# Kernel optimization log

Hardware: AMD Instinct MI355X
Metric: run time of the kernel (lower is better)

Reference implementation:

```python
import jax, jax.numpy as jnp
import numpy as np


def _seg_softmax(e, seg, n):
    m = jax.ops.segment_max(e, seg, num_segments=n)
    ex = jnp.exp(e - m[seg])
    s = jax.ops.segment_sum(ex, seg, num_segments=n)
    return ex / (s[seg] + 1e-16)


def _gat_conv(x, src, dst, ea, W, a_s, a_d, We, a_e, b, heads, C, concat, N):
    # PyG GATConv math (eval mode, no dropout)
    h = (x @ W).reshape(N, heads, C)                    # [N,H,C]
    he = (ea @ We).reshape(-1, heads, C)                # [Ef,H,C]
    al = jnp.sum(h * a_s, -1)[src] + jnp.sum(h * a_d, -1)[dst] + jnp.sum(he * a_e, -1)
    al = jax.nn.leaky_relu(al, 0.2)                     # [Ef,H]
    alpha = _seg_softmax(al, dst, N)
    out = jax.ops.segment_sum(alpha[:, :, None] * h[src], dst, num_segments=N)
    out = out.reshape(N, heads * C) if concat else out.mean(1)
    return out + b


def _ln(x, g, b):
    mu = x.mean(-1, keepdims=True)
    v = x.var(-1, keepdims=True)
    return (x - mu) / jnp.sqrt(v + 1e-5) * g + b


def setup_inputs() -> dict:
    key = jax.random.key(0)
    ks = jax.random.split(key, 20)
    B, L, E_PER = 512, 64, 4
    N = B * L
    E = N * E_PER
    x = jax.random.normal(ks[0], (N, 55), jnp.float32)
    # within-graph random edges (each graph is a contiguous block of L nodes)
    off = (jnp.arange(E) // (L * E_PER)) * L
    src = off + jax.random.randint(ks[1], (E,), 0, L)
    dst = off + jax.random.randint(ks[2], (E,), 0, L)
    edge_index = jnp.stack([src, dst])
    edge_attr = jax.random.uniform(ks[3], (E, 6), dtype=jnp.float32)
    node_gid = jnp.arange(N) // L
    food_ids = jax.random.randint(ks[4], (B,), 0, 29)
    p = lambda i, shape: jax.random.normal(ks[i], shape, jnp.float32) * 0.05
    return dict(
        x=x, edge_attr=edge_attr, edge_index=edge_index, node_gid=node_gid, food_ids=food_ids,
        W1=p(5, (55, 1024)), as1=p(6, (4, 256)), ad1=p(7, (4, 256)),
        We1=p(8, (6, 1024)), ae1=p(9, (4, 256)), b1=jnp.zeros((1024,), jnp.float32),
        g1=jnp.ones((1024,), jnp.float32), be1=jnp.zeros((1024,), jnp.float32),
        W2=p(10, (1024, 256)), as2=p(11, (1, 256)), ad2=p(12, (1, 256)),
        We2=p(13, (6, 256)), ae2=p(14, (1, 256)), b2=jnp.zeros((256,), jnp.float32),
        g2=jnp.ones((256,), jnp.float32), be2=jnp.zeros((256,), jnp.float32),
        Wa=p(15, (256, 256)), va=p(16, (256,)), emb=p(17, (29, 256)))


def reference(x, edge_attr, edge_index, node_gid, food_ids,
              W1, as1, ad1, We1, ae1, b1, g1, be1,
              W2, as2, ad2, We2, ae2, b2, g2, be2,
              Wa, va, emb):
    N = x.shape[0]
    B = food_ids.shape[0]
    src, dst = edge_index[0], edge_index[1]
    # add self loops; self-loop edge_attr = mean of incoming edge attrs (PyG fill_value='mean')
    ones = jnp.ones((src.shape[0],), x.dtype)
    deg = jax.ops.segment_sum(ones, dst, num_segments=N)
    mean_ea = jax.ops.segment_sum(edge_attr, dst, num_segments=N) / jnp.maximum(deg, 1.0)[:, None]
    loop = jnp.arange(N)
    src_f = jnp.concatenate([src, loop])
    dst_f = jnp.concatenate([dst, loop])
    ea_f = jnp.concatenate([edge_attr, mean_ea], 0)
    # GATEncoder
    h = _gat_conv(x, src_f, dst_f, ea_f, W1, as1, ad1, We1, ae1, b1, 4, 256, True, N)
    h = jax.nn.relu(_ln(h, g1, be1))
    h = _gat_conv(h, src_f, dst_f, ea_f, W2, as2, ad2, We2, ae2, b2, 1, 256, False, N)
    h = _ln(h, g2, be2)                                  # [N,256]
    # per-graph attention over nodes, then attention-weighted max-pool
    scores = jnp.tanh(h @ Wa) @ va                       # [N]
    attn = _seg_softmax(scores, node_gid, B)             # [N]
    hw = h * attn[:, None]
    drug_fea = jax.ops.segment_max(hw, node_gid, num_segments=B)[:, None, :]  # [B,1,256]
    food_fea = emb[food_ids][:, None, :]                 # [B,1,256]
    return drug_fea, food_fea, attn
```

## Files before the change

kernel.cpp:

```cpp
#include <hip/hip_runtime.h>
#include <cstdint>
#include <cstddef>


#define LEAKY_SLOPE 0.2f

typedef __attribute__((ext_vector_type(8))) _Float16 half8;
typedef __attribute__((ext_vector_type(4))) float facc4;

__global__ void k_prep_w(const float* __restrict__ W1, const float* __restrict__ W2,
                         const float* __restrict__ Wa,
                         const float* __restrict__ We1, const float* __restrict__ ae1,
                         const float* __restrict__ We2, const float* __restrict__ ae2,
                         const float* __restrict__ as1, const float* __restrict__ ad1,
                         _Float16* __restrict__ w1t, _Float16* __restrict__ w2t,
                         _Float16* __restrict__ wat, float* __restrict__ fold) {
    int idx = blockIdx.x * blockDim.x + threadIdx.x;
    if (idx < 1024 * 64) {
        int c = idx >> 6, k = idx & 63;
        w1t[idx] = (k < 55) ? (_Float16)W1[(size_t)k * 1024 + c] : (_Float16)0.f;
        return;
    }
    idx -= 1024 * 64;
    if (idx < 256 * 1024) {
        int c = idx >> 10, k = idx & 1023;
        w2t[idx] = (_Float16)W2[(size_t)k * 256 + c];
        return;
    }
    idx -= 256 * 1024;
    if (idx < 256 * 256) {
        int c = idx >> 8, k = idx & 255;
        int dst = ((c >> 4) * 8 + (k >> 5)) * 512 + ((c & 15) + 16 * ((k >> 3) & 3)) * 8 + (k & 7);
        wat[dst] = (_Float16)Wa[(size_t)k * 256 + c];
        return;
    }
    int t = idx - 256 * 256;
    if (t < 24) {
        int k = t >> 2, h = t & 3;
        float s = 0.f;
        for (int c = 0; c < 256; ++c) s += We1[k * 1024 + h * 256 + c] * ae1[h * 256 + c];
        fold[t] = s;
    } else if (t < 30) {
        int k = t - 24;
        float s = 0.f;
        for (int c = 0; c < 256; ++c) s += We2[k * 256 + c] * ae2[c];
        fold[32 + k] = s;
    } else if (t >= 64 && t < 284) {
        int i = t - 64, k = i >> 2, h = i & 3;
        float s = 0.f;
        for (int c = 0; c < 256; ++c) s += W1[k * 1024 + h * 256 + c] * as1[h * 256 + c];
        fold[64 + i] = s;
    } else if (t >= 320 && t < 540) {
        int i = t - 320, k = i >> 2, h = i & 3;
        float s = 0.f;
        for (int c = 0; c < 256; ++c) s += W1[k * 1024 + h * 256 + c] * ad1[h * 256 + c];
        fold[320 + i] = s;
    }
}

__global__ void k_prep_x(const float* __restrict__ x, const float* __restrict__ wa1,
                         const float* __restrict__ wd1, _Float16* __restrict__ xbf,
                         float* __restrict__ ss1, float* __restrict__ sd1, int N) {
    int idx = blockIdx.x * blockDim.x + threadIdx.x;
    if (idx < N * 64) {
        int n = idx >> 6, k = idx & 63;
        _Float16 v = (k < 55) ? (_Float16)x[(size_t)n * 55 + k] : (_Float16)0.f;
        int g = n >> 6, nl = n & 63;
        size_t dst = (size_t)g * 4096 +
                     (((k >> 4) * 2 + (nl >> 5)) * 512 +
                      ((k & 15) + 16 * ((nl >> 3) & 3)) * 8 + (nl & 7));
        xbf[dst] = v;
        return;
    }
    int n = idx - N * 64;
    if (n >= N) return;
    float a0 = 0, a1 = 0, a2 = 0, a3 = 0, d0 = 0, d1 = 0, d2 = 0, d3 = 0;
    for (int k = 0; k < 55; ++k) {
        float xv = x[(size_t)n * 55 + k];
        float4 wa = *reinterpret_cast<const float4*>(&wa1[k * 4]);
        float4 wd = *reinterpret_cast<const float4*>(&wd1[k * 4]);
        a0 += xv * wa.x; a1 += xv * wa.y; a2 += xv * wa.z; a3 += xv * wa.w;
        d0 += xv * wd.x; d1 += xv * wd.y; d2 += xv * wd.z; d3 += xv * wd.w;
    }
    *reinterpret_cast<float4*>(&ss1[n * 4]) = make_float4(a0, a1, a2, a3);
    *reinterpret_cast<float4*>(&sd1[n * 4]) = make_float4(d0, d1, d2, d3);
}

__global__ __launch_bounds__(256) void k_graph_csr(
    const int* __restrict__ ei, const float* __restrict__ ea,
    const float* __restrict__ we1, const float* __restrict__ we2,
    int* __restrict__ coff, int* __restrict__ eid,
    float* __restrict__ ead1, float* __restrict__ ead2, int E, int B) {
    __shared__ int degL[64];
    __shared__ float meaL[64][6];
    __shared__ int cs[65];
    __shared__ int fillL[64];
    int g = blockIdx.x;
    int ng = g * 64;
    int e0 = g * 256;
    int tid = threadIdx.x;
    if (tid < 64) {
        degL[tid] = 0; fillL[tid] = 0;
#pragma unroll
        for (int k = 0; k < 6; ++k) meaL[tid][k] = 0.f;
    }
    __syncthreads();
    int eg = e0 + tid;
    int dst = ei[E + eg];
    int dl = dst - ng;
    atomicAdd(&degL[dl], 1);
#pragma unroll
    for (int k = 0; k < 6; ++k) atomicAdd(&meaL[dl][k], ea[(size_t)eg * 6 + k]);
    __syncthreads();
    if (tid < 64) {
        int v = degL[tid] + 1;
        int incl = v;
#pragma unroll
        for (int o = 1; o < 64; o <<= 1) {
            int up = __shfl_up(incl, o);
            if (tid >= o) incl += up;
        }
        cs[tid + 1] = incl;
        if (tid == 0) cs[0] = 0;
        coff[ng + tid] = g * 320 + (incl - v);
        if (g == B - 1 && tid == 63) coff[ng + 64] = (g + 1) * 320;
    }
    __syncthreads();
    {
        float v[4] = {};
        float v2 = 0.f;
        const float* eap = ea + (size_t)eg * 6;
#pragma unroll
        for (int k = 0; k < 6; ++k) {
            float a = eap[k];
#pragma unroll
            for (int h = 0; h < 4; ++h) v[h] += a * we1[k * 4 + h];
            v2 += a * we2[k];
        }
#pragma unroll
        for (int h = 0; h < 4; ++h) ead1[(size_t)eg * 4 + h] = v[h];
        ead2[eg] = v2;
        int pos = cs[dl] + atomicAdd(&fillL[dl], 1);
        eid[g * 320 + pos] = eg;
    }
    if (tid < 64) {
        float inv = 1.f / fmaxf((float)degL[tid], 1.f);
        float v[4] = {};
        float v2 = 0.f;
#pragma unroll
        for (int k = 0; k < 6; ++k) {
            float a = meaL[tid][k] * inv;
#pragma unroll
            for (int h = 0; h < 4; ++h) v[h] += a * we1[k * 4 + h];
            v2 += a * we2[k];
        }
        int se = E + ng + tid;
#pragma unroll
        for (int h = 0; h < 4; ++h) ead1[(size_t)se * 4 + h] = v[h];
        ead2[se] = v2;
        int pos = cs[tid] + atomicAdd(&fillL[tid], 1);
        eid[g * 320 + pos] = se;
    }
}

__global__ __launch_bounds__(512) void k_pbuild1(
    const _Float16* __restrict__ xbf,
    const int* __restrict__ coff, const int* __restrict__ eid, const int* __restrict__ ei,
    const float* __restrict__ ead1, const float* __restrict__ ss1,
    const float* __restrict__ sd1,
    _Float16* __restrict__ XA, int ldxa, int E, int g0) {
    __shared__ _Float16 Pm[4][64 * 64];
    __shared__ float llds[384][4];
    __shared__ int slds[384];
    int g = blockIdx.x;
    int ng = (g0 + g) * 64;
    int lr0 = g * 64;
    int tid = threadIdx.x;
    int lane = tid & 63, wid = tid >> 6;
    int l15 = lane & 15, l4 = lane >> 4;
    for (int i = tid; i < 4 * 64 * 64 / 8; i += 512)
        *reinterpret_cast<int4*>(&Pm[0][0] + i * 8) = int4{0, 0, 0, 0};
    int pbase = coff[ng];
    int pcnt = coff[ng + 64] - pbase;
    if (pcnt > 384) pcnt = 384;
    for (int p = tid; p < pcnt; p += 512) {
        int e = eid[pbase + p];
        int s, d;
        if (e < E) { s = ei[e]; d = ei[E + e]; } else { s = e - E; d = s; }
        slds[p] = s - ng;
        float4 sv = *reinterpret_cast<const float4*>(&ss1[s * 4]);
        float4 dv = *reinterpret_cast<const float4*>(&sd1[d * 4]);
        float4 ev = *reinterpret_cast<const float4*>(&ead1[(size_t)e * 4]);
        float v0 = sv.x + dv.x + ev.x, v1 = sv.y + dv.y + ev.y;
        float v2 = sv.z + dv.z + ev.z, v3 = sv.w + dv.w + ev.w;
        llds[p][0] = (v0 > 0.f) ? v0 : LEAKY_SLOPE * v0;
        llds[p][1] = (v1 > 0.f) ? v1 : LEAKY_SLOPE * v1;
        llds[p][2] = (v2 > 0.f) ? v2 : LEAKY_SLOPE * v2;
        llds[p][3] = (v3 > 0.f) ? v3 : LEAKY_SLOPE * v3;
    }
    __syncthreads();
    if (tid < 256) {
        int dst = tid >> 2, h = tid & 3;
        int p0 = coff[ng + dst] - pbase, p1 = coff[ng + dst + 1] - pbase;
        float m = -1e30f;
        for (int p = p0; p < p1; ++p) m = fmaxf(m, llds[p][h]);
        float sm = 0.f;
        for (int p = p0; p < p1; ++p) sm += expf(llds[p][h] - m);
        float iv = 1.f / (sm + 1e-16f);
        for (int p = p0; p < p1; ++p) {
            int src = slds[p];
            int pos = dst * 64 + (((src >> 3) ^ (dst & 7)) << 3) + (src & 7);
            Pm[h][pos] = (_Float16)((float)Pm[h][pos] + expf(llds[p][h] - m) * iv);
        }
    }
    __syncthreads();
    int head = wid >> 1, fjh = wid & 1;
    const _Float16* xg = xbf + (size_t)(g0 + g) * 4096;
    facc4 acc[4][2] = {};
#pragma unroll
    for (int kk = 0; kk < 2; ++kk) {
        half8 af[4], bf[2];
#pragma unroll
        for (int f = 0; f < 4; ++f) {
            int arow = f * 16 + l15;
            af[f] = *reinterpret_cast<const half8*>(
                &Pm[head][arow * 64 + (((kk * 4 + l4) ^ (arow & 7)) << 3)]);
        }
#pragma unroll
        for (int f = 0; f < 2; ++f)
            bf[f] = *reinterpret_cast<const half8*>(
                xg + (((fjh * 2 + f) * 2 + kk) * 512 + lane * 8));
#pragma unroll
        for (int fi = 0; fi < 4; ++fi)
#pragma unroll
            for (int fj = 0; fj < 2; ++fj)
                acc[fi][fj] = __builtin_amdgcn_mfma_f32_16x16x32_f16(
                    af[fi], bf[fj], acc[fi][fj], 0, 0, 0);
    }
#pragma unroll
    for (int fi = 0; fi < 4; ++fi)
#pragma unroll
        for (int fj = 0; fj < 2; ++fj)
#pragma unroll
            for (int i = 0; i < 4; ++i) {
                int r = fi * 16 + l4 * 4 + i;
                int k2 = fjh * 32 + fj * 16 + l15;
                XA[((size_t)head * ldxa + lr0 + r) * 64 + k2] = (_Float16)acc[fi][fj][i];
            }
}

__global__ __launch_bounds__(256) void k_gemm_heads(
    const _Float16* __restrict__ XA, int ldxa, const _Float16* __restrict__ w1t,
    _Float16* __restrict__ hpre) {
    int h = blockIdx.z;
    const _Float16* A = XA + (size_t)h * ldxa * 64;
    const _Float16* BT = w1t + (size_t)h * 256 * 64;
    __shared__ _Float16 As[128 * 64];
    __shared__ _Float16 Bs[128 * 64];
    int tid = threadIdx.x;
    int lane = tid & 63, wid = tid >> 6;
    int wr = wid >> 1, wc = wid & 1;
    int l15 = lane & 15, l4 = lane >> 4;
    int r0 = blockIdx.y * 128, c0 = blockIdx.x * 128;
    facc4 acc[4][4] = {};
#pragma unroll
    for (int i = 0; i < 4; ++i) {
        int ch = tid + 256 * i;
        int row = ch >> 3, col16 = ch & 7;
        int sw = col16 ^ (row & 7);
        *reinterpret_cast<int4*>(&As[row * 64 + sw * 8]) =
            *reinterpret_cast<const int4*>(A + (size_t)(r0 + row) * 64 + col16 * 8);
        *reinterpret_cast<int4*>(&Bs[row * 64 + sw * 8]) =
            *reinterpret_cast<const int4*>(BT + (size_t)(c0 + row) * 64 + col16 * 8);
    }
    __syncthreads();
#pragma unroll
    for (int kk = 0; kk < 2; ++kk) {
        half8 af[4], bf[4];
#pragma unroll
        for (int f = 0; f < 4; ++f) {
            int arow = wr * 64 + f * 16 + l15;
            int ac = (kk * 4 + l4) ^ (arow & 7);
            af[f] = *reinterpret_cast<const half8*>(&As[arow * 64 + ac * 8]);
            int brow = wc * 64 + f * 16 + l15;
            int bc = (kk * 4 + l4) ^ (brow & 7);
            bf[f] = *reinterpret_cast<const half8*>(&Bs[brow * 64 + bc * 8]);
        }
#pragma unroll
        for (int fi = 0; fi < 4; ++fi)
#pragma unroll
            for (int fj = 0; fj < 4; ++fj)
                acc[fi][fj] = __builtin_amdgcn_mfma_f32_16x16x32_f16(
                    af[fi], bf[fj], acc[fi][fj], 0, 0, 0);
    }
#pragma unroll
    for (int fi = 0; fi < 4; ++fi)
#pragma unroll
        for (int fj = 0; fj < 4; ++fj)
#pragma unroll
            for (int i = 0; i < 4; ++i) {
                int r = r0 + wr * 64 + fi * 16 + l4 * 4 + i;
                int cc = h * 256 + c0 + wc * 64 + fj * 16 + l15;
                hpre[(size_t)r * 1024 + cc] = (_Float16)acc[fi][fj][i];
            }
}

__global__ __launch_bounds__(256) void k_ln1(
    const _Float16* __restrict__ hpre, const float* __restrict__ b1,
    const float* __restrict__ g1, const float* __restrict__ be1,
    _Float16* __restrict__ hln) {
    int row = blockIdx.x * 4 + (threadIdx.x >> 6);
    int lane = threadIdx.x & 63;
    const _Float16* src = hpre + (size_t)row * 1024;
    float v[16];
    half8 h0 = *reinterpret_cast<const half8*>(src + lane * 8);
    half8 h1 = *reinterpret_cast<const half8*>(src + 512 + lane * 8);
    float lsum = 0.f, lsq = 0.f;
#pragma unroll
    for (int j = 0; j < 8; ++j) {
        v[j] = (float)h0[j] + b1[lane * 8 + j];
        v[8 + j] = (float)h1[j] + b1[512 + lane * 8 + j];
    }
#pragma unroll
    for (int j = 0; j < 16; ++j) { lsum += v[j]; lsq += v[j] * v[j]; }
    for (int o = 32; o; o >>= 1) { lsum += __shfl_xor(lsum, o); lsq += __shfl_xor(lsq, o); }
    float mu = lsum * (1.f / 1024.f);
    float var = lsq * (1.f / 1024.f) - mu * mu;
    float rstd = rsqrtf(var + 1e-5f);
    half8 o0, o1;
#pragma unroll
    for (int j = 0; j < 8; ++j) {
        int c = lane * 8 + j;
        o0[j] = (_Float16)fmaxf((v[j] - mu) * rstd * g1[c] + be1[c], 0.f);
    }
#pragma unroll
    for (int j = 0; j < 8; ++j) {
        int c = 512 + lane * 8 + j;
        o1[j] = (_Float16)fmaxf((v[8 + j] - mu) * rstd * g1[c] + be1[c], 0.f);
    }
    *reinterpret_cast<half8*>(hln + (size_t)row * 1024 + lane * 8) = o0;
    *reinterpret_cast<half8*>(hln + (size_t)row * 1024 + 512 + lane * 8) = o1;
}

__global__ __launch_bounds__(512) void k_gemm2(
    const _Float16* __restrict__ A, const _Float16* __restrict__ BT,
    _Float16* __restrict__ h2f) {
    __shared__ _Float16 As[128 * 64];
    __shared__ _Float16 Bs[256 * 64];
    int tid = threadIdx.x;
    int lane = tid & 63, wid = tid >> 6;
    int wr = wid >> 2, wc = wid & 3;
    int l15 = lane & 15, l4 = lane >> 4;
    int r0 = blockIdx.x * 128;
    facc4 acc[4][4] = {};
    for (int kt = 0; kt < 1024; kt += 64) {
#pragma unroll
        for (int i = 0; i < 2; ++i) {
            int ch = tid + 512 * i;
            int row = ch >> 3, col16 = ch & 7;
            int sw = col16 ^ (row & 7);
            *reinterpret_cast<int4*>(&As[row * 64 + sw * 8]) =
                *reinterpret_cast<const int4*>(A + (size_t)(r0 + row) * 1024 + kt + col16 * 8);
        }
#pragma unroll
        for (int i = 0; i < 4; ++i) {
            int ch = tid + 512 * i;
            int row = ch >> 3, col16 = ch & 7;
            int sw = col16 ^ (row & 7);
            *reinterpret_cast<int4*>(&Bs[row * 64 + sw * 8]) =
                *reinterpret_cast<const int4*>(BT + (size_t)row * 1024 + kt + col16 * 8);
        }
        __syncthreads();
#pragma unroll
        for (int kk = 0; kk < 2; ++kk) {
            half8 af[4], bf[4];
#pragma unroll
            for (int f = 0; f < 4; ++f) {
                int arow = wr * 64 + f * 16 + l15;
                int ac = (kk * 4 + l4) ^ (arow & 7);
                af[f] = *reinterpret_cast<const half8*>(&As[arow * 64 + ac * 8]);
                int brow = wc * 64 + f * 16 + l15;
                int bc = (kk * 4 + l4) ^ (brow & 7);
                bf[f] = *reinterpret_cast<const half8*>(&Bs[brow * 64 + bc * 8]);
            }
#pragma unroll
            for (int fi = 0; fi < 4; ++fi)
#pragma unroll
                for (int fj = 0; fj < 4; ++fj)
                    acc[fi][fj] = __builtin_amdgcn_mfma_f32_16x16x32_f16(
                        af[fi], bf[fj], acc[fi][fj], 0, 0, 0);
        }
        __syncthreads();
    }
#pragma unroll
    for (int fi = 0; fi < 4; ++fi)
#pragma unroll
        for (int fj = 0; fj < 4; ++fj)
#pragma unroll
            for (int i = 0; i < 4; ++i) {
                int r = r0 + wr * 64 + fi * 16 + l4 * 4 + i;
                int cc = wc * 64 + fj * 16 + l15;
                int g = r >> 6, nl = r & 63;
                size_t dst = (size_t)g * 16384 +
                             (((cc >> 4) * 2 + (nl >> 5)) * 512 +
                              ((cc & 15) + 16 * ((nl >> 3) & 3)) * 8 + (nl & 7));
                h2f[dst] = (_Float16)acc[fi][fj][i];
            }
}

__global__ __launch_bounds__(512) void k_graph2f(
    const _Float16* __restrict__ h2f,
    const int* __restrict__ coff, const int* __restrict__ eid, const int* __restrict__ ei,
    const float* __restrict__ ead2, const float* __restrict__ as2,
    const float* __restrict__ ad2,
    const float* __restrict__ b2, const float* __restrict__ g2,
    const float* __restrict__ be2,
    const _Float16* __restrict__ wat, const float* __restrict__ va,
    const int* __restrict__ food, const float* __restrict__ emb,
    float* __restrict__ out, int E, int B, int g0) {
    __shared__ _Float16 hfL[64 * 256];
    _Float16* Pm = hfL;
    float* llds = reinterpret_cast<float*>(hfL + 4096);
    int* slds = reinterpret_cast<int*>(hfL + 4096 + 768);
    __shared__ float rsum[64], rsq[64], ss2L[64], sd2L[64];
    __shared__ float part[8][64];
    __shared__ float at[64];
    int g = blockIdx.x;
    int b = g0 + g;
    int ng = (g0 + g) * 64;
    int tid = threadIdx.x;
    int lane = tid & 63, wid = tid >> 6;
    int l15 = lane & 15, l4 = lane >> 4;
    int cbase = wid * 32;
    if (tid < 64) { rsum[tid] = 0.f; rsq[tid] = 0.f; ss2L[tid] = 0.f; sd2L[tid] = 0.f; }
    for (int i = tid; i < 64 * 64 / 8; i += 512)
        *reinterpret_cast<int4*>(&Pm[0] + i * 8) = int4{0, 0, 0, 0};
    __syncthreads();
    const _Float16* hg = h2f + (size_t)g * 16384;
    half8 bfr[2][2];
#pragma unroll
    for (int kk = 0; kk < 2; ++kk)
#pragma unroll
        for (int f = 0; f < 2; ++f)
            bfr[kk][f] = *reinterpret_cast<const half8*>(
                hg + ((((cbase + f * 16) >> 4) * 2 + kk) * 512 + lane * 8));
    float ps[2][8] = {}, pd[2][8] = {};
#pragma unroll
    for (int kk = 0; kk < 2; ++kk)
#pragma unroll
        for (int f = 0; f < 2; ++f) {
            int c = cbase + f * 16 + l15;
            float a2 = as2[c], d2 = ad2[c];
#pragma unroll
            for (int j = 0; j < 8; ++j) {
                float hv = (float)bfr[kk][f][j];
                ps[kk][j] += hv * a2;
                pd[kk][j] += hv * d2;
            }
        }
#pragma unroll
    for (int kk = 0; kk < 2; ++kk)
#pragma unroll
        for (int j = 0; j < 8; ++j) {
            float s = ps[kk][j], d = pd[kk][j];
            s += __shfl_xor(s, 1); d += __shfl_xor(d, 1);
            s += __shfl_xor(s, 2); d += __shfl_xor(d, 2);
            s += __shfl_xor(s, 4); d += __shfl_xor(d, 4);
            s += __shfl_xor(s, 8); d += __shfl_xor(d, 8);
            if (l15 == 0) {
                int n = kk * 32 + l4 * 8 + j;
                atomicAdd(&ss2L[n], s);
                atomicAdd(&sd2L[n], d);
            }
        }
    __syncthreads();
    int pbase = coff[ng];
    int pcnt = coff[ng + 64] - pbase;
    if (pcnt > 384) pcnt = 384;
    for (int p = tid; p < pcnt; p += 512) {
        int e = eid[pbase + p];
        int s, d;
        if (e < E) { s = ei[e]; d = ei[E + e]; } else { s = e - E; d = s; }
        slds[p] = s - ng;
        float v = ss2L[s - ng] + sd2L[d - ng] + ead2[e];
        llds[p] = (v > 0.f) ? v : LEAKY_SLOPE * v;
    }
    __syncthreads();
    if (tid < 64) {
        int dst = tid;
        int p0 = coff[ng + dst] - pbase, p1 = coff[ng + dst + 1] - pbase;
        float m = -1e30f;
        for (int p = p0; p < p1; ++p) m = fmaxf(m, llds[p]);
        float sm = 0.f;
        for (int p = p0; p < p1; ++p) sm += expf(llds[p] - m);
        float iv = 1.f / (sm + 1e-16f);
        for (int p = p0; p < p1; ++p) {
            int src = slds[p];
            int pos = dst * 64 + (((src >> 3) ^ (dst & 7)) << 3) + (src & 7);
            Pm[pos] = (_Float16)((float)Pm[pos] + expf(llds[p] - m) * iv);
        }
    }
    __syncthreads();
    facc4 acc[4][2] = {};
#pragma unroll
    for (int kk = 0; kk < 2; ++kk) {
        half8 af[4];
#pragma unroll
        for (int f = 0; f < 4; ++f) {
            int arow = f * 16 + l15;
            af[f] = *reinterpret_cast<const half8*>(
                &Pm[arow * 64 + (((kk * 4 + l4) ^ (arow & 7)) << 3)]);
        }
#pragma unroll
        for (int fi = 0; fi < 4; ++fi)
#pragma unroll
            for (int fj = 0; fj < 2; ++fj)
                acc[fi][fj] = __builtin_amdgcn_mfma_f32_16x16x32_f16(
                    af[fi], bfr[kk][fj], acc[fi][fj], 0, 0, 0);
    }
    float bb[2];
#pragma unroll
    for (int fj = 0; fj < 2; ++fj) bb[fj] = b2[cbase + fj * 16 + l15];
#pragma unroll
    for (int fi = 0; fi < 4; ++fi)
#pragma unroll
        for (int i = 0; i < 4; ++i) {
            float s = 0.f, q = 0.f;
#pragma unroll
            for (int fj = 0; fj < 2; ++fj) {
                float v = acc[fi][fj][i] + bb[fj];
                acc[fi][fj][i] = v;
                s += v; q += v * v;
            }
            s += __shfl_xor(s, 1); q += __shfl_xor(q, 1);
            s += __shfl_xor(s, 2); q += __shfl_xor(q, 2);
            s += __shfl_xor(s, 4); q += __shfl_xor(q, 4);
            s += __shfl_xor(s, 8); q += __shfl_xor(q, 8);
            if (l15 == 0) {
                int r = fi * 16 + l4 * 4 + i;
                atomicAdd(&rsum[r], s);
                atomicAdd(&rsq[r], q);
            }
        }
    __syncthreads();
#pragma unroll
    for (int fi = 0; fi < 4; ++fi)
#pragma unroll
        for (int i = 0; i < 4; ++i) {
            int rl = l4 * 4 + i;
            float mu = rsum[fi * 16 + rl] * (1.f / 256.f);
            float var = rsq[fi * 16 + rl] * (1.f / 256.f) - mu * mu;
            float rstd = rsqrtf(var + 1e-5f);
#pragma unroll
            for (int fj = 0; fj < 2; ++fj) {
                int c = cbase + fj * 16 + l15;
                float v = (acc[fi][fj][i] - mu) * rstd * g2[c] + be2[c];
                acc[fi][fj][i] = v;
                int idx = (fi * 8 + wid) * 512 +
                          ((fj * 2 + (l15 >> 3)) * 16 + rl) * 8 + (l15 & 7);
                hfL[idx] = (_Float16)v;
            }
        }
    __syncthreads();
    facc4 acc2[4][2] = {};
#pragma unroll
    for (int kk = 0; kk < 8; ++kk) {
        half8 af[4], bf[2];
#pragma unroll
        for (int f = 0; f < 4; ++f)
            af[f] = *reinterpret_cast<const half8*>(&hfL[(f * 8 + kk) * 512 + lane * 8]);
#pragma unroll
        for (int f = 0; f < 2; ++f)
            bf[f] = *reinterpret_cast<const half8*>(
                wat + (((wid * 2 + f) * 8 + kk) * 512 + lane * 8));
#pragma unroll
        for (int fi = 0; fi < 4; ++fi)
#pragma unroll
            for (int fj = 0; fj < 2; ++fj)
                acc2[fi][fj] = __builtin_amdgcn_mfma_f32_16x16x32_f16(
                    af[fi], bf[fj], acc2[fi][fj], 0, 0, 0);
    }
    float vac[2];
#pragma unroll
    for (int fj = 0; fj < 2; ++fj) vac[fj] = va[cbase + fj * 16 + l15];
#pragma unroll
    for (int fi = 0; fi < 4; ++fi)
#pragma unroll
        for (int i = 0; i < 4; ++i) {
            float v = tanhf(acc2[fi][0][i]) * vac[0] + tanhf(acc2[fi][1][i]) * vac[1];
            v += __shfl_xor(v, 1); v += __shfl_xor(v, 2);
            v += __shfl_xor(v, 4); v += __shfl_xor(v, 8);
            if (l15 == 0) part[wid][fi * 16 + l4 * 4 + i] = v;
        }
    __syncthreads();
    if (tid < 64) {
        float sc = part[0][tid] + part[1][tid] + part[2][tid] + part[3][tid] +
                   part[4][tid] + part[5][tid] + part[6][tid] + part[7][tid];
        float m = sc;
        for (int o = 32; o; o >>= 1) m = fmaxf(m, __shfl_xor(m, o));
        float ex = expf(sc - m);
        float s = ex;
        for (int o = 32; o; o >>= 1) s += __shfl_xor(s, o);
        float a = ex / (s + 1e-16f);
        at[tid] = a;
        out[(size_t)B * 512 + (size_t)b * 64 + tid] = a;
    }
    __syncthreads();
#pragma unroll
    for (int fj = 0; fj < 2; ++fj) {
        float m = -1e30f;
#pragma unroll
        for (int fi = 0; fi < 4; ++fi)
#pragma unroll
            for (int i = 0; i < 4; ++i) {
                int r = fi * 16 + l4 * 4 + i;
                m = fmaxf(m, acc[fi][fj][i] * at[r]);
            }
        m = fmaxf(m, __shfl_xor(m, 16));
        m = fmaxf(m, __shfl_xor(m, 32));
        if (l4 == 0)
            out[(size_t)b * 256 + cbase + fj * 16 + l15] = m;
    }
    if (tid < 256)
        out[(size_t)B * 256 + (size_t)b * 256 + tid] =
            emb[(size_t)food[b] * 256 + tid];
}

extern "C" void kernel_launch(void* const* d_in, const int* in_sizes, int n_in,
                              void* d_out, int out_size, void* d_ws, size_t ws_size,
                              hipStream_t stream) {
    const float* x   = (const float*)d_in[0];
    const float* ea  = (const float*)d_in[1];
    const int*   ei  = (const int*)d_in[2];
    const int*   food= (const int*)d_in[4];
    const float* W1  = (const float*)d_in[5];
    const float* as1 = (const float*)d_in[6];
    const float* ad1 = (const float*)d_in[7];
    const float* We1 = (const float*)d_in[8];
    const float* ae1 = (const float*)d_in[9];
    const float* b1  = (const float*)d_in[10];
    const float* g1  = (const float*)d_in[11];
    const float* be1 = (const float*)d_in[12];
    const float* W2  = (const float*)d_in[13];
    const float* as2 = (const float*)d_in[14];
    const float* ad2 = (const float*)d_in[15];
    const float* We2 = (const float*)d_in[16];
    const float* ae2 = (const float*)d_in[17];
    const float* b2  = (const float*)d_in[18];
    const float* g2  = (const float*)d_in[19];
    const float* be2 = (const float*)d_in[20];
    const float* Wa  = (const float*)d_in[21];
    const float* va  = (const float*)d_in[22];
    const float* emb = (const float*)d_in[23];
    float* out = (float*)d_out;

    const int N  = in_sizes[0] / 55;
    const int E  = in_sizes[2] / 2;
    const int B  = in_sizes[4];
    const int Ef = E + N;
    const int LPG = N / B;

    char* w = (char*)d_ws;
    size_t off = 0;
    auto take = [&](size_t bytes) -> char* {
        char* p = w + off;
        off = (off + bytes + 255) & ~(size_t)255;
        return p;
    };
    int*      coff = (int*)take((size_t)(N + 1) * 4);
    int*      eid  = (int*)take((size_t)Ef * 4);
    float*    ead1 = (float*)take((size_t)Ef * 4 * 4);
    float*    ead2 = (float*)take((size_t)Ef * 4);
    float*    fold = (float*)take(4096 * 4);
    float*    ss1  = (float*)take((size_t)N * 4 * 4);
    float*    sd1  = (float*)take((size_t)N * 4 * 4);
    _Float16* xbf  = (_Float16*)take((size_t)N * 64 * 2);
    _Float16* w1t  = (_Float16*)take((size_t)1024 * 64 * 2);
    _Float16* w2t  = (_Float16*)take((size_t)256 * 1024 * 2);
    _Float16* wat  = (_Float16*)take((size_t)256 * 256 * 2);
    size_t smallEnd = off;

    int G = B;
    while (G > 2 && smallEnd + (size_t)G * 32768 + 2ull * G * 131072 + 768 > ws_size) G >>= 1;
    _Float16* XA   = (_Float16*)take((size_t)G * 32768);
    _Float16* hpre = (_Float16*)take((size_t)G * 131072);
    _Float16* hln  = (_Float16*)take((size_t)G * 131072);
    _Float16* h2f  = (_Float16*)hpre;

    k_prep_w<<<(1024 * 64 + 256 * 1024 + 256 * 256 + 3072 + 255) / 256, 256, 0, stream>>>(
        W1, W2, Wa, We1, ae1, We2, ae2, as1, ad1, w1t, w2t, wat, fold);
    k_prep_x<<<(N * 64 + N + 255) / 256, 256, 0, stream>>>(
        x, fold + 64, fold + 320, xbf, ss1, sd1, N);
    k_graph_csr<<<B, 256, 0, stream>>>(ei, ea, fold, fold + 32, coff, eid,
                                       ead1, ead2, E, B);

    for (int g0 = 0; g0 < B; g0 += G) {
        int Gc = (g0 + G <= B) ? G : (B - g0);
        int NC = Gc * LPG;
        k_pbuild1<<<Gc, 512, 0, stream>>>(xbf, coff, eid, ei, ead1, ss1, sd1,
                                          XA, NC, E, g0);
        k_gemm_heads<<<dim3(2, NC / 128, 4), 256, 0, stream>>>(XA, NC, w1t, hpre);
        k_ln1<<<NC / 4, 256, 0, stream>>>(hpre, b1, g1, be1, hln);
        k_gemm2<<<NC / 128, 512, 0, stream>>>(hln, w2t, h2f);
        k_graph2f<<<Gc, 512, 0, stream>>>(h2f, coff, eid, ei, ead2, as2, ad2,
                                          b2, g2, be2, wat, va, food, emb,
                                          out, E, B, g0);
    }
}
```

Baseline: 150.8 us.

## Fuse layer-2 attention dot products into GEMM epilogue and parallelize edge softmax

The per-node source/destination attention scores for the second GAT layer are now computed in the k_gemm2 epilogue from fp32 accumulators and written to global buffers, instead of being recomputed from fp16 h in k_graph2f. The per-graph softmax, previously done serially by 64 threads, now uses 8 threads per destination with shuffle reductions, followed by a parallel per-edge scatter into an fp32 LDS matrix via atomics, then a conversion to fp16. This removes serial per-destination loops and redundant dot products, at the cost of extra global traffic, LDS atomics and more barriers.

Result: no change. 151.8 us (+0.6%).

```diff
diff --git a/kernel.cpp b/kernel.cpp
--- a/kernel.cpp
+++ b/kernel.cpp
@@ -344,14 +344,18 @@
 
 __global__ __launch_bounds__(512) void k_gemm2(
     const _Float16* __restrict__ A, const _Float16* __restrict__ BT,
-    _Float16* __restrict__ h2f) {
+    const float* __restrict__ as2, const float* __restrict__ ad2,
+    _Float16* __restrict__ h2f, float* __restrict__ ss2, float* __restrict__ sd2,
+    int n0) {
     __shared__ _Float16 As[128 * 64];
     __shared__ _Float16 Bs[256 * 64];
+    __shared__ float s2L[128], d2L[128];
     int tid = threadIdx.x;
     int lane = tid & 63, wid = tid >> 6;
     int wr = wid >> 2, wc = wid & 3;
     int l15 = lane & 15, l4 = lane >> 4;
     int r0 = blockIdx.x * 128;
+    if (tid < 128) { s2L[tid] = 0.f; d2L[tid] = 0.f; }
     facc4 acc[4][4] = {};
     for (int kt = 0; kt < 1024; kt += 64) {
 #pragma unroll
@@ -395,24 +399,43 @@
 #pragma unroll
     for (int fi = 0; fi < 4; ++fi)
 #pragma unroll
-        for (int fj = 0; fj < 4; ++fj)
-#pragma unroll
-            for (int i = 0; i < 4; ++i) {
+        for (int i = 0; i < 4; ++i) {
+            float s2 = 0.f, d2 = 0.f;
+#pragma unroll
+            for (int fj = 0; fj < 4; ++fj) {
                 int r = r0 + wr * 64 + fi * 16 + l4 * 4 + i;
                 int cc = wc * 64 + fj * 16 + l15;
+                float v = acc[fi][fj][i];
                 int g = r >> 6, nl = r & 63;
                 size_t dst = (size_t)g * 16384 +
                              (((cc >> 4) * 2 + (nl >> 5)) * 512 +
                               ((cc & 15) + 16 * ((nl >> 3) & 3)) * 8 + (nl & 7));
-                h2f[dst] = (_Float16)acc[fi][fj][i];
-            }
+                h2f[dst] = (_Float16)v;
+                s2 += v * as2[cc];
+                d2 += v * ad2[cc];
+            }
+            s2 += __shfl_xor(s2, 1); d2 += __shfl_xor(d2, 1);
+            s2 += __shfl_xor(s2, 2); d2 += __shfl_xor(d2, 2);
+            s2 += __shfl_xor(s2, 4); d2 += __shfl_xor(d2, 4);
+            s2 += __shfl_xor(s2, 8); d2 += __shfl_xor(d2, 8);
+            if (l15 == 0) {
+                int rl = wr * 64 + fi * 16 + l4 * 4 + i;
+                atomicAdd(&s2L[rl], s2);
+                atomicAdd(&d2L[rl], d2);
+            }
+        }
+    __syncthreads();
+    if (tid < 128) {
+        ss2[n0 + r0 + tid] = s2L[tid];
+        sd2[n0 + r0 + tid] = d2L[tid];
+    }
 }
 
 __global__ __launch_bounds__(512) void k_graph2f(
     const _Float16* __restrict__ h2f,
     const int* __restrict__ coff, const int* __restrict__ eid, const int* __restrict__ ei,
-    const float* __restrict__ ead2, const float* __restrict__ as2,
-    const float* __restrict__ ad2,
+    const float* __restrict__ ead2, const float* __restrict__ ss2g,
+    const float* __restrict__ sd2g,
     const float* __restrict__ b2, const float* __restrict__ g2,
     const float* __restrict__ be2,
     const _Float16* __restrict__ wat, const float* __restrict__ va,
@@ -420,9 +443,13 @@
     float* __restrict__ out, int E, int B, int g0) {
     __shared__ _Float16 hfL[64 * 256];
     _Float16* Pm = hfL;
-    float* llds = reinterpret_cast<float*>(hfL + 4096);
-    int* slds = reinterpret_cast<int*>(hfL + 4096 + 768);
-    __shared__ float rsum[64], rsq[64], ss2L[64], sd2L[64];
+    float* Pf = reinterpret_cast<float*>(hfL + 4096);
+    float* llds = reinterpret_cast<float*>(hfL + 12288);
+    int* slds = reinterpret_cast<int*>(hfL + 12288 + 640);
+    int* dlds = reinterpret_cast<int*>(hfL + 12288 + 1280);
+    float* mL  = reinterpret_cast<float*>(hfL + 12288 + 1920);
+    float* ivL = reinterpret_cast<float*>(hfL + 12288 + 2048);
+    __shared__ float rsum[64], rsq[64];
     __shared__ float part[8][64];
     __shared__ float at[64];
     int g = blockIdx.x;
@@ -432,10 +459,9 @@
     int lane = tid & 63, wid = tid >> 6;
     int l15 = lane & 15, l4 = lane >> 4;
     int cbase = wid * 32;
-    if (tid < 64) { rsum[tid] = 0.f; rsq[tid] = 0.f; ss2L[tid] = 0.f; sd2L[tid] = 0.f; }
-    for (int i = tid; i < 64 * 64 / 8; i += 512)
-        *reinterpret_cast<int4*>(&Pm[0] + i * 8) = int4{0, 0, 0, 0};
-    __syncthreads();
+    if (tid < 64) { rsum[tid] = 0.f; rsq[tid] = 0.f; }
+    for (int i = tid; i < 1024; i += 512)
+        reinterpret_cast<int4*>(Pf)[i] = int4{0, 0, 0, 0};
     const _Float16* hg = h2f + (size_t)g * 16384;
     half8 bfr[2][2];
 #pragma unroll
@@ -444,36 +470,6 @@
         for (int f = 0; f < 2; ++f)
             bfr[kk][f] = *reinterpret_cast<const half8*>(
                 hg + ((((cbase + f * 16) >> 4) * 2 + kk) * 512 + lane * 8));
-    float ps[2][8] = {}, pd[2][8] = {};
-#pragma unroll
-    for (int kk = 0; kk < 2; ++kk)
-#pragma unroll
-        for (int f = 0; f < 2; ++f) {
-            int c = cbase + f * 16 + l15;
-            float a2 = as2[c], d2 = ad2[c];
-#pragma unroll
-            for (int j = 0; j < 8; ++j) {
-                float hv = (float)bfr[kk][f][j];
-                ps[kk][j] += hv * a2;
-                pd[kk][j] += hv * d2;
-            }
-        }
-#pragma unroll
-    for (int kk = 0; kk < 2; ++kk)
-#pragma unroll
-        for (int j = 0; j < 8; ++j) {
-            float s = ps[kk][j], d = pd[kk][j];
-            s += __shfl_xor(s, 1); d += __shfl_xor(d, 1);
-            s += __shfl_xor(s, 2); d += __shfl_xor(d, 2);
-            s += __shfl_xor(s, 4); d += __shfl_xor(d, 4);
-            s += __shfl_xor(s, 8); d += __shfl_xor(d, 8);
-            if (l15 == 0) {
-                int n = kk * 32 + l4 * 8 + j;
-                atomicAdd(&ss2L[n], s);
-                atomicAdd(&sd2L[n], d);
-            }
-        }
-    __syncthreads();
     int pbase = coff[ng];
     int pcnt = coff[ng + 64] - pbase;
     if (pcnt > 384) pcnt = 384;
@@ -482,23 +478,42 @@
         int s, d;
         if (e < E) { s = ei[e]; d = ei[E + e]; } else { s = e - E; d = s; }
         slds[p] = s - ng;
-        float v = ss2L[s - ng] + sd2L[d - ng] + ead2[e];
+        dlds[p] = d - ng;
+        float v = ss2g[s] + sd2g[d] + ead2[e];
         llds[p] = (v > 0.f) ? v : LEAKY_SLOPE * v;
     }
     __syncthreads();
-    if (tid < 64) {
-        int dst = tid;
+    {
+        int dst = tid >> 3, sub = tid & 7;
         int p0 = coff[ng + dst] - pbase, p1 = coff[ng + dst + 1] - pbase;
         float m = -1e30f;
-        for (int p = p0; p < p1; ++p) m = fmaxf(m, llds[p]);
+        for (int p = p0 + sub; p < p1; p += 8) m = fmaxf(m, llds[p]);
+        m = fmaxf(m, __shfl_xor(m, 1));
+        m = fmaxf(m, __shfl_xor(m, 2));
+        m = fmaxf(m, __shfl_xor(m, 4));
         float sm = 0.f;
-        for (int p = p0; p < p1; ++p) sm += expf(llds[p] - m);
-        float iv = 1.f / (sm + 1e-16f);
-        for (int p = p0; p < p1; ++p) {
-            int src = slds[p];
-            int pos = dst * 64 + (((src >> 3) ^ (dst & 7)) << 3) + (src & 7);
-            Pm[pos] = (_Float16)((float)Pm[pos] + expf(llds[p] - m) * iv);
-        }
+        for (int p = p0 + sub; p < p1; p += 8) sm += expf(llds[p] - m);
+        sm += __shfl_xor(sm, 1);
+        sm += __shfl_xor(sm, 2);
+        sm += __shfl_xor(sm, 4);
+        if (sub == 0) { mL[dst] = m; ivL[dst] = 1.f / (sm + 1e-16f); }
+    }
+    __syncthreads();
+    for (int p = tid; p < pcnt; p += 512) {
+        int d = dlds[p];
+        int src = slds[p];
+        float a = expf(llds[p] - mL[d]) * ivL[d];
+        atomicAdd(&Pf[d * 64 + (((src >> 3) ^ (d & 7)) << 3) + (src & 7)], a);
+    }
+    __syncthreads();
+    {
+        float4 a = reinterpret_cast<const float4*>(Pf)[tid * 2];
+        float4 c = reinterpret_cast<const float4*>(Pf)[tid * 2 + 1];
+        half8 o;
+        o[0] = (_Float16)a.x; o[1] = (_Float16)a.y; o[2] = (_Float16)a.z; o[3] = (_Float16)a.w;
+        o[4] = (_Float16)c.x; o[5] = (_Float16)c.y; o[6] = (_Float16)c.z; o[7] = (_Float16)c.w;
+        __syncthreads();
+        *reinterpret_cast<half8*>(&Pm[tid * 8]) = o;
     }
     __syncthreads();
     facc4 acc[4][2] = {};
@@ -674,6 +689,8 @@
     float*    fold = (float*)take(4096 * 4);
     float*    ss1  = (float*)take((size_t)N * 4 * 4);
     float*    sd1  = (float*)take((size_t)N * 4 * 4);
+    float*    ss2  = (float*)take((size_t)N * 4);
+    float*    sd2  = (float*)take((size_t)N * 4);
     _Float16* xbf  = (_Float16*)take((size_t)N * 64 * 2);
     _Float16* w1t  = (_Float16*)take((size_t)1024 * 64 * 2);
     _Float16* w2t  = (_Float16*)take((size_t)256 * 1024 * 2);
@@ -696,13 +713,14 @@
 
     for (int g0 = 0; g0 < B; g0 += G) {
         int Gc = (g0 + G <= B) ? G : (B - g0);
+        int n0 = g0 * LPG;
         int NC = Gc * LPG;
         k_pbuild1<<<Gc, 512, 0, stream>>>(xbf, coff, eid, ei, ead1, ss1, sd1,
                                           XA, NC, E, g0);
         k_gemm_heads<<<dim3(2, NC / 128, 4), 256, 0, stream>>>(XA, NC, w1t, hpre);
         k_ln1<<<NC / 4, 256, 0, stream>>>(hpre, b1, g1, be1, hln);
-        k_gemm2<<<NC / 128, 512, 0, stream>>>(hln, w2t, h2f);
-        k_graph2f<<<Gc, 512, 0, stream>>>(h2f, coff, eid, ei, ead2, as2, ad2,
+        k_gemm2<<<NC / 128, 512, 0, stream>>>(hln, w2t, as2, ad2, h2f, ss2, sd2, n0);
+        k_graph2f<<<Gc, 512, 0, stream>>>(h2f, coff, eid, ei, ead2, ss2, sd2,
                                           b2, g2, be2, wat, va, food, emb,
                                           out, E, B, g0);
     }
```

## Fuse layer-1 aggregation and per-head W1 GEMM into one kernel

Applied to the files above, without the earlier changes.

Merges the attention-weighted aggregation kernel and the per-head W1 GEMM into a single per-graph kernel. The aggregated 64x64 per-head tile stays in shared memory in MFMA fragment layout instead of going through a global XA buffer. W1 is pre-packed into fragment order so B fragments load straight from global memory. This removes one launch and the XA write/read round trip, at the cost of more accumulator registers (32 acc tiles per wave) and W1 being re-read per graph block.

Result: no change. 148.5 us (median of 2 runs) (-1.5%).

```diff
diff --git a/kernel.cpp b/kernel.cpp
--- a/kernel.cpp
+++ b/kernel.cpp
@@ -13,12 +13,18 @@
                          const float* __restrict__ We1, const float* __restrict__ ae1,
                          const float* __restrict__ We2, const float* __restrict__ ae2,
                          const float* __restrict__ as1, const float* __restrict__ ad1,
-                         _Float16* __restrict__ w1t, _Float16* __restrict__ w2t,
+                         _Float16* __restrict__ w1f, _Float16* __restrict__ w2t,
                          _Float16* __restrict__ wat, float* __restrict__ fold) {
     int idx = blockIdx.x * blockDim.x + threadIdx.x;
     if (idx < 1024 * 64) {
-        int c = idx >> 6, k = idx & 63;
-        w1t[idx] = (k < 55) ? (_Float16)W1[(size_t)k * 1024 + c] : (_Float16)0.f;
+        int head = idx >> 14;
+        int rem = idx & 16383;
+        int c = rem >> 6, k = rem & 63;
+        _Float16 v = (k < 55) ? (_Float16)W1[(size_t)k * 1024 + head * 256 + c]
+                              : (_Float16)0.f;
+        int dst = head * 16384 + ((c >> 4) * 2 + (k >> 5)) * 512 +
+                  ((c & 15) + 16 * ((k >> 3) & 3)) * 8 + (k & 7);
+        w1f[dst] = v;
         return;
     }
     idx -= 1024 * 64;
@@ -163,22 +169,23 @@
     }
 }
 
-__global__ __launch_bounds__(512) void k_pbuild1(
+__global__ __launch_bounds__(512) void k_layer1(
     const _Float16* __restrict__ xbf,
     const int* __restrict__ coff, const int* __restrict__ eid, const int* __restrict__ ei,
     const float* __restrict__ ead1, const float* __restrict__ ss1,
     const float* __restrict__ sd1,
-    _Float16* __restrict__ XA, int ldxa, int E, int g0) {
-    __shared__ _Float16 Pm[4][64 * 64];
+    const _Float16* __restrict__ w1f, _Float16* __restrict__ hpre,
+    int E, int g0) {
+    __shared__ _Float16 Pm[4][4096];
     __shared__ float llds[384][4];
     __shared__ int slds[384];
+    _Float16* XAf = &Pm[0][0];
     int g = blockIdx.x;
     int ng = (g0 + g) * 64;
-    int lr0 = g * 64;
     int tid = threadIdx.x;
     int lane = tid & 63, wid = tid >> 6;
     int l15 = lane & 15, l4 = lane >> 4;
-    for (int i = tid; i < 4 * 64 * 64 / 8; i += 512)
+    for (int i = tid; i < 4 * 4096 / 8; i += 512)
         *reinterpret_cast<int4*>(&Pm[0][0] + i * 8) = int4{0, 0, 0, 0};
     int pbase = coff[ng];
     int pcnt = coff[ng + 64] - pbase;
@@ -216,7 +223,7 @@
     __syncthreads();
     int head = wid >> 1, fjh = wid & 1;
     const _Float16* xg = xbf + (size_t)(g0 + g) * 4096;
-    facc4 acc[4][2] = {};
+    facc4 acc1[4][2] = {};
 #pragma unroll
     for (int kk = 0; kk < 2; ++kk) {
         half8 af[4], bf[2];
@@ -234,74 +241,51 @@
         for (int fi = 0; fi < 4; ++fi)
 #pragma unroll
             for (int fj = 0; fj < 2; ++fj)
-                acc[fi][fj] = __builtin_amdgcn_mfma_f32_16x16x32_f16(
-                    af[fi], bf[fj], acc[fi][fj], 0, 0, 0);
-    }
+                acc1[fi][fj] = __builtin_amdgcn_mfma_f32_16x16x32_f16(
+                    af[fi], bf[fj], acc1[fi][fj], 0, 0, 0);
+    }
+    __syncthreads();
 #pragma unroll
     for (int fi = 0; fi < 4; ++fi)
 #pragma unroll
         for (int fj = 0; fj < 2; ++fj)
 #pragma unroll
             for (int i = 0; i < 4; ++i) {
-                int r = fi * 16 + l4 * 4 + i;
-                int k2 = fjh * 32 + fj * 16 + l15;
-                XA[((size_t)head * ldxa + lr0 + r) * 64 + k2] = (_Float16)acc[fi][fj][i];
-            }
-}
-
-__global__ __launch_bounds__(256) void k_gemm_heads(
-    const _Float16* __restrict__ XA, int ldxa, const _Float16* __restrict__ w1t,
-    _Float16* __restrict__ hpre) {
-    int h = blockIdx.z;
-    const _Float16* A = XA + (size_t)h * ldxa * 64;
-    const _Float16* BT = w1t + (size_t)h * 256 * 64;
-    __shared__ _Float16 As[128 * 64];
-    __shared__ _Float16 Bs[128 * 64];
-    int tid = threadIdx.x;
-    int lane = tid & 63, wid = tid >> 6;
-    int wr = wid >> 1, wc = wid & 1;
-    int l15 = lane & 15, l4 = lane >> 4;
-    int r0 = blockIdx.y * 128, c0 = blockIdx.x * 128;
-    facc4 acc[4][4] = {};
-#pragma unroll
-    for (int i = 0; i < 4; ++i) {
-        int ch = tid + 256 * i;
-        int row = ch >> 3, col16 = ch & 7;
-        int sw = col16 ^ (row & 7);
-        *reinterpret_cast<int4*>(&As[row * 64 + sw * 8]) =
-            *reinterpret_cast<const int4*>(A + (size_t)(r0 + row) * 64 + col16 * 8);
-        *reinterpret_cast<int4*>(&Bs[row * 64 + sw * 8]) =
-            *reinterpret_cast<const int4*>(BT + (size_t)(c0 + row) * 64 + col16 * 8);
-    }
-    __syncthreads();
+                int rl = l4 * 4 + i;
+                int dst = head * 4096 + (fi * 2 + fjh) * 512 +
+                          ((fj * 2 + (l15 >> 3)) * 16 + rl) * 8 + (l15 & 7);
+                XAf[dst] = (_Float16)acc1[fi][fj][i];
+            }
+    __syncthreads();
+    int hw = wid >> 1, ch = wid & 1;
+    facc4 acc2[4][8] = {};
 #pragma unroll
     for (int kk = 0; kk < 2; ++kk) {
-        half8 af[4], bf[4];
-#pragma unroll
-        for (int f = 0; f < 4; ++f) {
-            int arow = wr * 64 + f * 16 + l15;
-            int ac = (kk * 4 + l4) ^ (arow & 7);
-            af[f] = *reinterpret_cast<const half8*>(&As[arow * 64 + ac * 8]);
-            int brow = wc * 64 + f * 16 + l15;
-            int bc = (kk * 4 + l4) ^ (brow & 7);
-            bf[f] = *reinterpret_cast<const half8*>(&Bs[brow * 64 + bc * 8]);
-        }
+        half8 af[4], bf[8];
+#pragma unroll
+        for (int f = 0; f < 4; ++f)
+            af[f] = *reinterpret_cast<const half8*>(
+                &XAf[hw * 4096 + (f * 2 + kk) * 512 + lane * 8]);
+#pragma unroll
+        for (int f = 0; f < 8; ++f)
+            bf[f] = *reinterpret_cast<const half8*>(
+                w1f + hw * 16384 + ((ch * 8 + f) * 2 + kk) * 512 + lane * 8);
 #pragma unroll
         for (int fi = 0; fi < 4; ++fi)
 #pragma unroll
-            for (int fj = 0; fj < 4; ++fj)
-                acc[fi][fj] = __builtin_amdgcn_mfma_f32_16x16x32_f16(
-                    af[fi], bf[fj], acc[fi][fj], 0, 0, 0);
+            for (int fj = 0; fj < 8; ++fj)
+                acc2[fi][fj] = __builtin_amdgcn_mfma_f32_16x16x32_f16(
+                    af[fi], bf[fj], acc2[fi][fj], 0, 0, 0);
     }
 #pragma unroll
     for (int fi = 0; fi < 4; ++fi)
 #pragma unroll
-        for (int fj = 0; fj < 4; ++fj)
+        for (int fj = 0; fj < 8; ++fj)
 #pragma unroll
             for (int i = 0; i < 4; ++i) {
-                int r = r0 + wr * 64 + fi * 16 + l4 * 4 + i;
-                int cc = h * 256 + c0 + wc * 64 + fj * 16 + l15;
-                hpre[(size_t)r * 1024 + cc] = (_Float16)acc[fi][fj][i];
+                int r = g * 64 + fi * 16 + l4 * 4 + i;
+                int cc = hw * 256 + ch * 128 + fj * 16 + l15;
+                hpre[(size_t)r * 1024 + cc] = (_Float16)acc2[fi][fj][i];
             }
 }
 
@@ -675,20 +659,19 @@
     float*    ss1  = (float*)take((size_t)N * 4 * 4);
     float*    sd1  = (float*)take((size_t)N * 4 * 4);
     _Float16* xbf  = (_Float16*)take((size_t)N * 64 * 2);
-    _Float16* w1t  = (_Float16*)take((size_t)1024 * 64 * 2);
+    _Float16* w1f  = (_Float16*)take((size_t)1024 * 64 * 2);
     _Float16* w2t  = (_Float16*)take((size_t)256 * 1024 * 2);
     _Float16* wat  = (_Float16*)take((size_t)256 * 256 * 2);
     size_t smallEnd = off;
 
     int G = B;
-    while (G > 2 && smallEnd + (size_t)G * 32768 + 2ull * G * 131072 + 768 > ws_size) G >>= 1;
-    _Float16* XA   = (_Float16*)take((size_t)G * 32768);
+    while (G > 2 && smallEnd + 2ull * G * 131072 + 768 > ws_size) G >>= 1;
     _Float16* hpre = (_Float16*)take((size_t)G * 131072);
     _Float16* hln  = (_Float16*)take((size_t)G * 131072);
     _Float16* h2f  = (_Float16*)hpre;
 
     k_prep_w<<<(1024 * 64 + 256 * 1024 + 256 * 256 + 3072 + 255) / 256, 256, 0, stream>>>(
-        W1, W2, Wa, We1, ae1, We2, ae2, as1, ad1, w1t, w2t, wat, fold);
+        W1, W2, Wa, We1, ae1, We2, ae2, as1, ad1, w1f, w2t, wat, fold);
     k_prep_x<<<(N * 64 + N + 255) / 256, 256, 0, stream>>>(
         x, fold + 64, fold + 320, xbf, ss1, sd1, N);
     k_graph_csr<<<B, 256, 0, stream>>>(ei, ea, fold, fold + 32, coff, eid,
@@ -697,9 +680,8 @@
     for (int g0 = 0; g0 < B; g0 += G) {
         int Gc = (g0 + G <= B) ? G : (B - g0);
         int NC = Gc * LPG;
-        k_pbuild1<<<Gc, 512, 0, stream>>>(xbf, coff, eid, ei, ead1, ss1, sd1,
-                                          XA, NC, E, g0);
-        k_gemm_heads<<<dim3(2, NC / 128, 4), 256, 0, stream>>>(XA, NC, w1t, hpre);
+        k_layer1<<<Gc, 512, 0, stream>>>(xbf, coff, eid, ei, ead1, ss1, sd1,
+                                         w1f, hpre, E, g0);
         k_ln1<<<NC / 4, 256, 0, stream>>>(hpre, b1, g1, be1, hln);
         k_gemm2<<<NC / 128, 512, 0, stream>>>(hln, w2t, h2f);
         k_graph2f<<<Gc, 512, 0, stream>>>(h2f, coff, eid, ei, ead2, as2, ad2,
```
